# Kernel optimization log

Measured on AMD Instinct MI355X. Metric: run time of the kernel, lower is better.

## Reference

```python
import jax, jax.numpy as jnp
import numpy as np

N = 50000      # nodes
E = 1600000    # edges (avg degree 32)
F_IN = 512     # in_channels
H = 128        # hidden_channels


def setup_inputs() -> dict:
    key = jax.random.key(0)
    k0, k1, k2, k3 = jax.random.split(key, 4)
    x = jax.random.normal(k0, (N, F_IN), dtype=jnp.float32)
    edge_index = jax.random.randint(k1, (2, E), 0, N, dtype=jnp.int32)
    edge_weight = jnp.ones((E,), dtype=jnp.float32)
    # GCNConv weight (glorot) + bias, Linear weight (xavier) + bias.
    # Stored as [in, out] for direct matmul (same math as torch's x @ W.T).
    W_conv = jax.random.normal(k2, (F_IN, H), dtype=jnp.float32) * np.sqrt(2.0 / (F_IN + H)).astype(np.float32)
    b_conv = jnp.zeros((H,), dtype=jnp.float32)
    W_lin = jax.random.normal(k3, (H, F_IN), dtype=jnp.float32) * np.sqrt(2.0 / (H + F_IN)).astype(np.float32)
    b_lin = jnp.zeros((F_IN,), dtype=jnp.float32)
    return {
        "x": x, "edge_index": edge_index, "edge_weight": edge_weight,
        "W_conv": W_conv, "b_conv": b_conv, "W_lin": W_lin, "b_lin": b_lin,
    }


def reference(x, edge_index, edge_weight, W_conv, b_conv, W_lin, b_lin):
    n = x.shape[0]
    src, dst = edge_index[0], edge_index[1]
    # GCN normalization with self-loops (add_self_loops + sym norm)
    loop = jnp.arange(n, dtype=edge_index.dtype)
    src_f = jnp.concatenate([src, loop])            # [E+N]
    dst_f = jnp.concatenate([dst, loop])
    w = jnp.concatenate([edge_weight, jnp.ones((n,), x.dtype)])
    deg = jax.ops.segment_sum(w, dst_f, num_segments=n)  # [N]
    dinv = jnp.where(deg > 0, jax.lax.rsqrt(deg), 0.0)
    norm = dinv[src_f] * w * dinv[dst_f]            # [E+N]
    # GCNConv: transform then normalized neighbor aggregation
    h = x @ W_conv                                  # [N, H]
    agg = jax.ops.segment_sum(h[src_f] * norm[:, None], dst_f, num_segments=n) + b_conv  # [N, H]
    # dropout p=0.0 (eval) is identity; final linear projection back to F_IN
    return agg @ W_lin + b_lin                      # [N, F_IN]
```

## Files before the change

kernel.cpp:

```cpp
#include <hip/hip_runtime.h>

#define NN 50000
#define EE 1600000
#define FIN 512
#define HH 128

#define CAP 80
#define OVF_CAP 64512

#define GROUP 128
#define NB ((NN + GROUP - 1) / GROUP)
#define NBLK 256
#define EPB (EE / NBLK)

typedef short s16x8 __attribute__((ext_vector_type(8)));
typedef float f32x4 __attribute__((ext_vector_type(4)));

static __device__ inline unsigned short f2bf(float f) {
    unsigned u = __float_as_uint(f);
    unsigned r = (u + 0x7fffu + ((u >> 16) & 1u)) >> 16;
    return (unsigned short)r;
}

static __device__ inline float blo(unsigned u) { return __uint_as_float(u << 16); }
static __device__ inline float bhi(unsigned u) { return __uint_as_float(u & 0xffff0000u); }


__global__ __launch_bounds__(256) void hist_kernel(const int* __restrict__ dst,
                                                   int* __restrict__ hist) {
    __shared__ int h[NB];
    const int tid = threadIdx.x;
    for (int i = tid; i < NB; i += 256) h[i] = 0;
    __syncthreads();
    const int base = blockIdx.x * EPB;
    for (int i = tid; i < EPB; i += 256)
        atomicAdd(&h[dst[base + i] >> 7], 1);
    __syncthreads();
    for (int i = tid; i < NB; i += 256) hist[blockIdx.x * NB + i] = h[i];
}

__global__ __launch_bounds__(64) void scan_bins(const int* __restrict__ hist,
                                                int* __restrict__ off,
                                                int* __restrict__ binTotal) {
    const int bin = blockIdx.x;
    const int lane = threadIdx.x;
    int v[4];
    int s = 0;
#pragma unroll
    for (int i = 0; i < 4; ++i) { v[i] = hist[(lane * 4 + i) * NB + bin]; s += v[i]; }
    int incl = s;
#pragma unroll
    for (int d = 1; d < 64; d <<= 1) {
        int t = __shfl_up(incl, d, 64);
        if (lane >= d) incl += t;
    }
    int run = incl - s;
#pragma unroll
    for (int i = 0; i < 4; ++i) { off[(lane * 4 + i) * NB + bin] = run; run += v[i]; }
    if (lane == 63) binTotal[bin] = incl;
}

__global__ __launch_bounds__(512) void bin_base(const int* __restrict__ binTotal,
                                                int* __restrict__ binBase) {
    __shared__ int s[512];
    const int t = threadIdx.x;
    int mine = (t < NB) ? binTotal[t] : 0;
    s[t] = mine;
    __syncthreads();
    for (int d = 1; d < 512; d <<= 1) {
        int v = (t >= d) ? s[t - d] : 0;
        __syncthreads();
        s[t] += v;
        __syncthreads();
    }
    if (t < NB) binBase[t] = s[t] - mine;
}

__global__ __launch_bounds__(256) void place_kernel(const int* __restrict__ src,
                                                    const int* __restrict__ dst,
                                                    const float* __restrict__ w,
                                                    const int* __restrict__ off,
                                                    const int* __restrict__ binBase,
                                                    int2* __restrict__ bins) {
    __shared__ int cur[NB];
    const int tid = threadIdx.x;
    for (int i = tid; i < NB; i += 256)
        cur[i] = binBase[i] + off[blockIdx.x * NB + i];
    __syncthreads();
    const int base = blockIdx.x * EPB;
    for (int i = tid; i < EPB; i += 256) {
        int e = base + i;
        int s = src[e], d = dst[e];
        float we = w[e];
        int pos = atomicAdd(&cur[d >> 7], 1);
        bins[pos] = make_int2(s | ((d & 127) << 16), __float_as_int(we));
    }
}

__global__ __launch_bounds__(512) void bucket_build(const int* __restrict__ binBase,
                                                    const int* __restrict__ binTotal,
                                                    const int2* __restrict__ bins,
                                                    int* __restrict__ cnt,
                                                    int2* __restrict__ bucket,
                                                    float* __restrict__ deg,
                                                    int* __restrict__ ovf_cnt,
                                                    int4* __restrict__ ovf) {
    __shared__ int lcnt[GROUP];
    __shared__ float lw[GROUP];
    const int b = blockIdx.x;
    const int tid = threadIdx.x;
    if (tid < GROUP) { lcnt[tid] = 0; lw[tid] = 0.0f; }
    __syncthreads();
    const int base = b * GROUP;
    const int start = binBase[b];
    const int n = binTotal[b];
    for (int i = tid; i < n; i += 512) {
        int2 en = bins[start + i];
        int sr = en.x & 0xffff;
        int dl = (en.x >> 16) & 127;
        int pos = atomicAdd(&lcnt[dl], 1);
        if (pos < CAP) {
            bucket[(size_t)(base + dl) * CAP + pos] = make_int2(sr, en.y);
            atomicAdd(&lw[dl], __int_as_float(en.y));
        } else {
            int o = atomicAdd(ovf_cnt, 1);
            if (o < OVF_CAP) ovf[o] = make_int4(sr, base + dl, en.y, 0);
        }
    }
    __syncthreads();
    for (int i = tid; i < GROUP; i += 512) {
        int node = base + i;
        if (node < NN) {
            cnt[node] = lcnt[i];
            deg[node] = 1.0f + lw[i];
        }
    }
}

__global__ void ovf_deg(const int* __restrict__ ovf_cnt, const int4* __restrict__ ovf,
                        float* __restrict__ deg) {
    int n = min(*ovf_cnt, OVF_CAP);
    for (int i = blockIdx.x * blockDim.x + threadIdx.x; i < n; i += blockDim.x * gridDim.x)
        atomicAdd(deg + ovf[i].y, __int_as_float(ovf[i].z));
}

__global__ void dinv_kernel(const float* __restrict__ deg, float* __restrict__ dinv, int n) {
    int i = blockIdx.x * 256 + threadIdx.x;
    if (i < n) {
        float d = deg[i];
        dinv[i] = (d > 0.0f) ? rsqrtf(d) : 0.0f;
    }
}


__global__ __launch_bounds__(256) void gemm1_kernel(const float* __restrict__ A,
                                                    const float* __restrict__ B,
                                                    const float* __restrict__ dinv,
                                                    unsigned short* __restrict__ h2,
                                                    int M) {
    __shared__ short As[128][40];
    __shared__ short Bs[128][40];
    const int bm = blockIdx.x * 128;
    const int tid = threadIdx.x;
    const int wave = tid >> 6, lane = tid & 63;
    const int wm = wave >> 1, wn = wave & 1;
    const int mlane = lane & 15, quad = lane >> 4;

    f32x4 acc[4][4];
#pragma unroll
    for (int i = 0; i < 4; ++i)
#pragma unroll
        for (int j = 0; j < 4; ++j) acc[i][j] = (f32x4){0.f, 0.f, 0.f, 0.f};

    for (int k0 = 0; k0 < FIN; k0 += 32) {
#pragma unroll
        for (int i = 0; i < 4; ++i) {
            int task = tid + i * 256;
            int row = task >> 3, kq = task & 7;
            int grow = bm + row;
            float4 v = make_float4(0.f, 0.f, 0.f, 0.f);
            if (grow < M) v = *(const float4*)(A + (size_t)grow * FIN + k0 + kq * 4);
            ushort4 b;
            b.x = f2bf(v.x); b.y = f2bf(v.y); b.z = f2bf(v.z); b.w = f2bf(v.w);
            *(ushort4*)&As[row][kq * 4] = b;
        }
#pragma unroll
        for (int i = 0; i < 2; ++i) {
            int task = tid + i * 256;
            int n = task & 127, kg = task >> 7;
            unsigned short tmp[8];
#pragma unroll
            for (int j = 0; j < 8; ++j)
                tmp[j] = f2bf(B[(size_t)(k0 + kg * 8 + j) * HH + n]);
            *(s16x8*)&Bs[n][kg * 8] = *(s16x8*)tmp;
        }
        __syncthreads();

        s16x8 af[4], bfr[4];
#pragma unroll
        for (int mt = 0; mt < 4; ++mt)
            af[mt] = *(const s16x8*)&As[wm * 64 + mt * 16 + mlane][quad * 8];
#pragma unroll
        for (int nt = 0; nt < 4; ++nt)
            bfr[nt] = *(const s16x8*)&Bs[wn * 64 + nt * 16 + mlane][quad * 8];
#pragma unroll
        for (int mt = 0; mt < 4; ++mt)
#pragma unroll
            for (int nt = 0; nt < 4; ++nt)
                acc[mt][nt] = __builtin_amdgcn_mfma_f32_16x16x32_bf16(af[mt], bfr[nt], acc[mt][nt], 0, 0, 0);
        __syncthreads();
    }

#pragma unroll
    for (int mt = 0; mt < 4; ++mt) {
#pragma unroll
        for (int r = 0; r < 4; ++r) {
            int row = bm + wm * 64 + mt * 16 + quad * 4 + r;
            if (row < M) {
                float sc = dinv[row];
#pragma unroll
                for (int nt = 0; nt < 4; ++nt) {
                    int col = wn * 64 + nt * 16 + mlane;
                    h2[(size_t)row * HH + col] = f2bf(acc[mt][nt][r] * sc);
                }
            }
        }
    }
}


__global__ __launch_bounds__(256) void agg_kernel(const unsigned int* __restrict__ h2u,
                                                  const int* __restrict__ cnt,
                                                  const int2* __restrict__ bucket,
                                                  const float* __restrict__ dinv,
                                                  const float* __restrict__ b_conv,
                                                  const int* __restrict__ ovf_cnt,
                                                  const int4* __restrict__ ovf,
                                                  unsigned int* __restrict__ aggu, int n) {
    int idx = blockIdx.x * 256 + threadIdx.x;
    int node = idx >> 6;
    int lane = idx & 63;
    if (node >= n) return;
    int c = min(cnt[node], CAP);
    const int2* e = bucket + (size_t)node * CAP;

    unsigned self = h2u[(size_t)node * 64 + lane];
    float a0 = blo(self), a1 = bhi(self);
    float b0 = 0.0f, b1 = 0.0f;

    int j = 0;
    for (; j + 8 <= c; j += 8) {
        int4 p0 = *(const int4*)(e + j);
        int4 p1 = *(const int4*)(e + j + 2);
        int4 p2 = *(const int4*)(e + j + 4);
        int4 p3 = *(const int4*)(e + j + 6);
        unsigned u0 = h2u[(size_t)p0.x * 64 + lane];
        unsigned u1 = h2u[(size_t)p0.z * 64 + lane];
        unsigned u2 = h2u[(size_t)p1.x * 64 + lane];
        unsigned u3 = h2u[(size_t)p1.z * 64 + lane];
        unsigned u4 = h2u[(size_t)p2.x * 64 + lane];
        unsigned u5 = h2u[(size_t)p2.z * 64 + lane];
        unsigned u6 = h2u[(size_t)p3.x * 64 + lane];
        unsigned u7 = h2u[(size_t)p3.z * 64 + lane];
        float w0 = __int_as_float(p0.y), w1 = __int_as_float(p0.w);
        float w2 = __int_as_float(p1.y), w3 = __int_as_float(p1.w);
        float w4 = __int_as_float(p2.y), w5 = __int_as_float(p2.w);
        float w6 = __int_as_float(p3.y), w7 = __int_as_float(p3.w);
        a0 += w0 * blo(u0); a1 += w0 * bhi(u0);
        b0 += w1 * blo(u1); b1 += w1 * bhi(u1);
        a0 += w2 * blo(u2); a1 += w2 * bhi(u2);
        b0 += w3 * blo(u3); b1 += w3 * bhi(u3);
        a0 += w4 * blo(u4); a1 += w4 * bhi(u4);
        b0 += w5 * blo(u5); b1 += w5 * bhi(u5);
        a0 += w6 * blo(u6); a1 += w6 * bhi(u6);
        b0 += w7 * blo(u7); b1 += w7 * bhi(u7);
    }
    for (; j + 2 <= c; j += 2) {
        int4 p = *(const int4*)(e + j);
        unsigned u0 = h2u[(size_t)p.x * 64 + lane];
        unsigned u1 = h2u[(size_t)p.z * 64 + lane];
        float w0 = __int_as_float(p.y), w1 = __int_as_float(p.w);
        a0 += w0 * blo(u0); a1 += w0 * bhi(u0);
        b0 += w1 * blo(u1); b1 += w1 * bhi(u1);
    }
    if (j < c) {
        int2 p = e[j];
        float w0 = __int_as_float(p.y);
        unsigned u0 = h2u[(size_t)p.x * 64 + lane];
        a0 += w0 * blo(u0); a1 += w0 * bhi(u0);
    }

    int ovf_n = min(*ovf_cnt, OVF_CAP);
    for (int i = 0; i < ovf_n; ++i) {
        int4 v = ovf[i];
        if (v.y == node) {
            float w0 = __int_as_float(v.z);
            unsigned u0 = h2u[(size_t)v.x * 64 + lane];
            a0 += w0 * blo(u0); a1 += w0 * bhi(u0);
        }
    }

    float di = dinv[node];
    float2 bc = *(const float2*)&b_conv[lane * 2];
    float v0 = bc.x + di * (a0 + b0);
    float v1 = bc.y + di * (a1 + b1);
    aggu[(size_t)node * 64 + lane] = (unsigned)f2bf(v0) | ((unsigned)f2bf(v1) << 16);
}


__global__ __launch_bounds__(256) void gemm2_kernel(const unsigned short* __restrict__ A,
                                                    const float* __restrict__ B,
                                                    const float* __restrict__ bias,
                                                    float* __restrict__ C,
                                                    int M) {
    __shared__ short As[128][40];
    __shared__ short Bs[128][40];
    const int bm = blockIdx.x * 128;
    const int bn = blockIdx.y * 128;
    const int tid = threadIdx.x;
    const int wave = tid >> 6, lane = tid & 63;
    const int wm = wave >> 1, wn = wave & 1;
    const int mlane = lane & 15, quad = lane >> 4;

    f32x4 acc[4][4];
#pragma unroll
    for (int i = 0; i < 4; ++i)
#pragma unroll
        for (int j = 0; j < 4; ++j) acc[i][j] = (f32x4){0.f, 0.f, 0.f, 0.f};

    for (int k0 = 0; k0 < HH; k0 += 32) {
#pragma unroll
        for (int i = 0; i < 2; ++i) {
            int task = tid + i * 256;
            int row = task >> 2, ch = task & 3;
            int grow = bm + row;
            s16x8 v = (s16x8){0, 0, 0, 0, 0, 0, 0, 0};
            if (grow < M) v = *(const s16x8*)(A + (size_t)grow * HH + k0 + ch * 8);
            *(s16x8*)&As[row][ch * 8] = v;
        }
#pragma unroll
        for (int i = 0; i < 2; ++i) {
            int task = tid + i * 256;
            int n = task & 127, kg = task >> 7;
            unsigned short tmp[8];
#pragma unroll
            for (int j = 0; j < 8; ++j)
                tmp[j] = f2bf(B[(size_t)(k0 + kg * 8 + j) * FIN + bn + n]);
            *(s16x8*)&Bs[n][kg * 8] = *(s16x8*)tmp;
        }
        __syncthreads();

        s16x8 af[4], bfr[4];
#pragma unroll
        for (int mt = 0; mt < 4; ++mt)
            af[mt] = *(const s16x8*)&As[wm * 64 + mt * 16 + mlane][quad * 8];
#pragma unroll
        for (int nt = 0; nt < 4; ++nt)
            bfr[nt] = *(const s16x8*)&Bs[wn * 64 + nt * 16 + mlane][quad * 8];
#pragma unroll
        for (int mt = 0; mt < 4; ++mt)
#pragma unroll
            for (int nt = 0; nt < 4; ++nt)
                acc[mt][nt] = __builtin_amdgcn_mfma_f32_16x16x32_bf16(af[mt], bfr[nt], acc[mt][nt], 0, 0, 0);
        __syncthreads();
    }

#pragma unroll
    for (int mt = 0; mt < 4; ++mt) {
#pragma unroll
        for (int r = 0; r < 4; ++r) {
            int row = bm + wm * 64 + mt * 16 + quad * 4 + r;
            if (row < M) {
#pragma unroll
                for (int nt = 0; nt < 4; ++nt) {
                    int col = bn + wn * 64 + nt * 16 + mlane;
                    C[(size_t)row * FIN + col] = acc[mt][nt][r] + bias[col];
                }
            }
        }
    }
}


extern "C" void kernel_launch(void* const* d_in, const int* in_sizes, int n_in,
                              void* d_out, int out_size, void* d_ws, size_t ws_size,
                              hipStream_t stream) {
    const float* x      = (const float*)d_in[0];
    const int*   ei     = (const int*)d_in[1];
    const float* ew     = (const float*)d_in[2];
    const float* W_conv = (const float*)d_in[3];
    const float* b_conv = (const float*)d_in[4];
    const float* W_lin  = (const float*)d_in[5];
    const float* b_lin  = (const float*)d_in[6];
    float* out = (float*)d_out;

    const int* src = ei;
    const int* dst = ei + EE;

    char* ws = (char*)d_ws;
    int*            cnt      = (int*)           (ws + 0);
    float*          deg      = (float*)         (ws + 200704);
    float*          dinv     = (float*)         (ws + 401408);
    int*            ovf_cnt  = (int*)           (ws + 602112);
    int*            binTotal = (int*)           (ws + 602368);
    int*            binBase  = (int*)           (ws + 604160);
    int4*           ovf      = (int4*)          (ws + 605952);
    int2*           bucket   = (int2*)          (ws + 1650944);
    unsigned short* h2       = (unsigned short*)(ws + 33650944);
    unsigned short* agg      = (unsigned short*)(ws + 46450944);

    int*            hist     = (int*)           (ws + 1650944);
    int*            off      = (int*)           (ws + 2051584);
    int2*           bins     = (int2*)          (ws + 33650944);

    hipMemsetAsync(ovf_cnt, 0, sizeof(int), stream);

    const int nb_n = (NN + 255) / 256;
    const int nb_w = (NN * 64 + 255) / 256;

    hist_kernel<<<NBLK, 256, 0, stream>>>(dst, hist);
    scan_bins<<<NB, 64, 0, stream>>>(hist, off, binTotal);
    bin_base<<<1, 512, 0, stream>>>(binTotal, binBase);
    place_kernel<<<NBLK, 256, 0, stream>>>(src, dst, ew, off, binBase, bins);
    bucket_build<<<NB, 512, 0, stream>>>(binBase, binTotal, bins, cnt, bucket, deg, ovf_cnt, ovf);
    ovf_deg<<<4, 256, 0, stream>>>(ovf_cnt, ovf, deg);
    dinv_kernel<<<nb_n, 256, 0, stream>>>(deg, dinv, NN);

    gemm1_kernel<<<dim3((NN + 127) / 128, 1), 256, 0, stream>>>(x, W_conv, dinv, h2, NN);

    agg_kernel<<<nb_w, 256, 0, stream>>>((const unsigned int*)h2, cnt, bucket, dinv, b_conv,
                                         ovf_cnt, ovf, (unsigned int*)agg, NN);

    gemm2_kernel<<<dim3((NN + 127) / 128, FIN / 128), 256, 0, stream>>>(agg, W_lin, b_lin, out, NN);
}
```

Baseline: 374.0 us.

## Double-buffer gemm1 global loads in registers and use 512-thread blocks

The first GEMM now runs 8 waves per block, each computing a 32x64 tile instead of 64x64. Global loads for the next K-slices are issued into two register buffers before the MFMA work on the current slice, so memory latency overlaps compute. The cost is more register pressure from the prefetch buffers and an extra barrier per K step.

```diff
diff --git a/kernel.cpp b/kernel.cpp
--- a/kernel.cpp
+++ b/kernel.cpp
@@ -153,7 +153,7 @@
 }
 
 
-__global__ __launch_bounds__(256) void gemm1_kernel(const float* __restrict__ A,
+__global__ __launch_bounds__(512) void gemm1_kernel(const float* __restrict__ A,
                                                     const float* __restrict__ B,
                                                     const float* __restrict__ dinv,
                                                     unsigned short* __restrict__ h2,
@@ -166,56 +166,76 @@
     const int wm = wave >> 1, wn = wave & 1;
     const int mlane = lane & 15, quad = lane >> 4;
 
-    f32x4 acc[4][4];
-#pragma unroll
-    for (int i = 0; i < 4; ++i)
+    const int ar = tid >> 3, akq = tid & 7;
+    const int bn = tid & 127, bkg = tid >> 7;
+
+    f32x4 acc[2][4];
+#pragma unroll
+    for (int i = 0; i < 2; ++i)
 #pragma unroll
         for (int j = 0; j < 4; ++j) acc[i][j] = (f32x4){0.f, 0.f, 0.f, 0.f};
 
-    for (int k0 = 0; k0 < FIN; k0 += 32) {
-#pragma unroll
-        for (int i = 0; i < 4; ++i) {
-            int task = tid + i * 256;
-            int row = task >> 3, kq = task & 7;
-            int grow = bm + row;
-            float4 v = make_float4(0.f, 0.f, 0.f, 0.f);
-            if (grow < M) v = *(const float4*)(A + (size_t)grow * FIN + k0 + kq * 4);
+    float4 pa0[2], pa1[2];
+    float pb0[8], pb1[8];
+
+    auto loadT = [&](float4 (&pa)[2], float (&pb)[8], int k0) {
+#pragma unroll
+        for (int i = 0; i < 2; ++i) {
+            int grow = bm + ar + i * 64;
+            pa[i] = make_float4(0.f, 0.f, 0.f, 0.f);
+            if (grow < M) pa[i] = *(const float4*)(A + (size_t)grow * FIN + k0 + akq * 4);
+        }
+#pragma unroll
+        for (int j = 0; j < 8; ++j)
+            pb[j] = B[(size_t)(k0 + bkg * 8 + j) * HH + bn];
+    };
+    auto storeT = [&](float4 (&pa)[2], float (&pb)[8]) {
+#pragma unroll
+        for (int i = 0; i < 2; ++i) {
             ushort4 b;
-            b.x = f2bf(v.x); b.y = f2bf(v.y); b.z = f2bf(v.z); b.w = f2bf(v.w);
-            *(ushort4*)&As[row][kq * 4] = b;
-        }
-#pragma unroll
-        for (int i = 0; i < 2; ++i) {
-            int task = tid + i * 256;
-            int n = task & 127, kg = task >> 7;
-            unsigned short tmp[8];
-#pragma unroll
-            for (int j = 0; j < 8; ++j)
-                tmp[j] = f2bf(B[(size_t)(k0 + kg * 8 + j) * HH + n]);
-            *(s16x8*)&Bs[n][kg * 8] = *(s16x8*)tmp;
-        }
-        __syncthreads();
-
-        s16x8 af[4], bfr[4];
-#pragma unroll
-        for (int mt = 0; mt < 4; ++mt)
-            af[mt] = *(const s16x8*)&As[wm * 64 + mt * 16 + mlane][quad * 8];
+            b.x = f2bf(pa[i].x); b.y = f2bf(pa[i].y); b.z = f2bf(pa[i].z); b.w = f2bf(pa[i].w);
+            *(ushort4*)&As[ar + i * 64][akq * 4] = b;
+        }
+        unsigned short tmp[8];
+#pragma unroll
+        for (int j = 0; j < 8; ++j) tmp[j] = f2bf(pb[j]);
+        *(s16x8*)&Bs[bn][bkg * 8] = *(s16x8*)tmp;
+    };
+    auto mmaT = [&]() {
+        s16x8 af[2], bfr[4];
+#pragma unroll
+        for (int mt = 0; mt < 2; ++mt)
+            af[mt] = *(const s16x8*)&As[wm * 32 + mt * 16 + mlane][quad * 8];
 #pragma unroll
         for (int nt = 0; nt < 4; ++nt)
             bfr[nt] = *(const s16x8*)&Bs[wn * 64 + nt * 16 + mlane][quad * 8];
 #pragma unroll
-        for (int mt = 0; mt < 4; ++mt)
+        for (int mt = 0; mt < 2; ++mt)
 #pragma unroll
             for (int nt = 0; nt < 4; ++nt)
                 acc[mt][nt] = __builtin_amdgcn_mfma_f32_16x16x32_bf16(af[mt], bfr[nt], acc[mt][nt], 0, 0, 0);
-        __syncthreads();
-    }
-
-#pragma unroll
-    for (int mt = 0; mt < 4; ++mt) {
+    };
+
+    loadT(pa0, pb0, 0);
+    loadT(pa1, pb1, 32);
+    for (int kk = 0; kk < 16; kk += 2) {
+        storeT(pa0, pb0);
+        __syncthreads();
+        if (kk + 2 < 16) loadT(pa0, pb0, (kk + 2) * 32);
+        mmaT();
+        __syncthreads();
+        storeT(pa1, pb1);
+        __syncthreads();
+        if (kk + 3 < 16) loadT(pa1, pb1, (kk + 3) * 32);
+        mmaT();
+        __syncthreads();
+    }
+
+#pragma unroll
+    for (int mt = 0; mt < 2; ++mt) {
 #pragma unroll
         for (int r = 0; r < 4; ++r) {
-            int row = bm + wm * 64 + mt * 16 + quad * 4 + r;
+            int row = bm + wm * 32 + mt * 16 + quad * 4 + r;
             if (row < M) {
                 float sc = dinv[row];
 #pragma unroll
@@ -426,7 +446,7 @@
     ovf_deg<<<4, 256, 0, stream>>>(ovf_cnt, ovf, deg);
     dinv_kernel<<<nb_n, 256, 0, stream>>>(deg, dinv, NN);
 
-    gemm1_kernel<<<dim3((NN + 127) / 128, 1), 256, 0, stream>>>(x, W_conv, dinv, h2, NN);
+    gemm1_kernel<<<dim3((NN + 127) / 128, 1), 512, 0, stream>>>(x, W_conv, dinv, h2, NN);
 
     agg_kernel<<<nb_w, 256, 0, stream>>>((const unsigned int*)h2, cnt, bucket, dinv, b_conv,
                                          ovf_cnt, ovf, (unsigned int*)agg, NN);
```

Result: faster. 354.0 us (-5.4%).
